# Optimization experiments

Hardware: AMD Instinct MI355X
Metric: run time of the kernel (lower is better)

Reference implementation:

```python
import jax, jax.numpy as jnp
import numpy as np

NUM_USERS = 100000
NUM_ITEMS = 50000
N_TOTAL = NUM_USERS + NUM_ITEMS
NNZ = 4000000
LATENT_DIM = 64
N_LAYERS = 3
BATCH = 16384


def setup_inputs() -> dict:
    key = jax.random.key(0)
    k1, k2, k3, k4, k5, k6, k7 = jax.random.split(key, 7)
    return {
        "user_emb": jax.random.normal(k1, (NUM_USERS, LATENT_DIM), dtype=jnp.float32) * 0.1,
        "item_emb": jax.random.normal(k2, (NUM_ITEMS, LATENT_DIM), dtype=jnp.float32) * 0.1,
        "vals": jax.random.uniform(k3, (NNZ,), dtype=jnp.float32),
        "rows": jax.random.randint(k4, (NNZ,), 0, N_TOTAL, dtype=jnp.int32),
        "cols": jax.random.randint(k5, (NNZ,), 0, N_TOTAL, dtype=jnp.int32),
        "users": jax.random.randint(k6, (BATCH,), 0, NUM_USERS, dtype=jnp.int64),
        "items": jax.random.randint(k7, (BATCH,), 0, NUM_ITEMS, dtype=jnp.int64),
    }


def _spmm(vals, rows, cols, x):
    # sparse.mm(A, x) with A given as COO edge list: out[r] += vals * x[c]
    return jax.ops.segment_sum(vals[:, None] * x[cols], rows, num_segments=N_TOTAL)


def reference(user_emb, item_emb, vals, rows, cols, users, items):
    # LightGCN.computer(): multi-hop propagation + mean over layer outputs
    all_emb = jnp.concatenate([user_emb, item_emb], axis=0)  # [N+M, d]
    acc = all_emb
    emb = all_emb
    for _ in range(N_LAYERS):
        emb = _spmm(vals, rows, cols, emb)
        acc = acc + emb
    light_out = acc / jnp.asarray(N_LAYERS + 1, dtype=acc.dtype)
    all_users = light_out[:NUM_USERS]
    all_items = light_out[NUM_USERS:]
    # forward(users, items): gather and elementwise dot product
    u = all_users[users]  # [B, d]
    i = all_items[items]  # [B, d]
    gamma = jnp.sum(u * i, axis=1)  # [B]
    return gamma
```

## Files before the change

kernel.cpp:

```cpp
#include <hip/hip_runtime.h>

#define NUM_USERS 100000
#define NUM_ITEMS 50000
#define N_TOTAL   150000
#define LATENT    64
#define BATCH     16384
#define BROWS     512
#define NB        293

typedef unsigned int u32;
typedef unsigned short u16;

__device__ __forceinline__ u16 f32_to_bf16(float f) {
    u32 u = __float_as_uint(f);
    u32 r = (u + 0x7FFFu + ((u >> 16) & 1u)) >> 16;
    return (u16)r;
}
__device__ __forceinline__ float bf16_lo(u32 w) { return __uint_as_float(w << 16); }
__device__ __forceinline__ float bf16_hi(u32 w) { return __uint_as_float(w & 0xFFFF0000u); }

__global__ void coarse_hist_kernel(const int* __restrict__ rows, int* __restrict__ ccnt, int nnz) {
    __shared__ int h[NB];
    for (int i = threadIdx.x; i < NB; i += blockDim.x) h[i] = 0;
    __syncthreads();
    int stride = gridDim.x * blockDim.x;
    for (int e = blockIdx.x * blockDim.x + threadIdx.x; e < nnz; e += stride)
        atomicAdd(&h[rows[e] >> 9], 1);
    __syncthreads();
    for (int i = threadIdx.x; i < NB; i += blockDim.x)
        if (h[i]) atomicAdd(&ccnt[i], h[i]);
}

__global__ void coarse_scan_kernel(const int* __restrict__ ccnt, int* __restrict__ cptr,
                                   int* __restrict__ ccur, int* __restrict__ rowptr, int nnz) {
    __shared__ int s[512];
    int t = threadIdx.x;
    int v = (t < NB) ? ccnt[t] : 0;
    s[t] = v;
    __syncthreads();
    for (int d = 1; d < 512; d <<= 1) {
        int x = (t >= d) ? s[t - d] : 0;
        __syncthreads();
        s[t] += x;
        __syncthreads();
    }
    int excl = s[t] - v;
    if (t < NB) { cptr[t] = excl; ccur[t] = excl; }
    if (t == 0) { cptr[NB] = nnz; rowptr[N_TOTAL] = nnz; }
}

__global__ void partition1_kernel(const int* __restrict__ rows, const int* __restrict__ cols,
                                  const float* __restrict__ vals,
                                  int* __restrict__ ccur, uint2* __restrict__ packed0, int nnz) {
    __shared__ int lh[NB];
    __shared__ int lc[NB];
    int t = threadIdx.x;
    for (int i = t; i < NB; i += blockDim.x) lh[i] = 0;
    __syncthreads();
    int epb = (nnz + gridDim.x - 1) / gridDim.x;
    int s0 = blockIdx.x * epb;
    int s1 = s0 + epb; if (s1 > nnz) s1 = nnz;
    for (int e = s0 + t; e < s1; e += blockDim.x)
        atomicAdd(&lh[rows[e] >> 9], 1);
    __syncthreads();
    for (int i = t; i < NB; i += blockDim.x) {
        int c = lh[i];
        lc[i] = c ? atomicAdd(&ccur[i], c) : 0;
    }
    __syncthreads();
    for (int e = s0 + t; e < s1; e += blockDim.x) {
        int r = rows[e];
        int pos = atomicAdd(&lc[r >> 9], 1);
        packed0[pos] = make_uint2((u32)cols[e] | ((u32)(r & (BROWS - 1)) << 18),
                                  __float_as_uint(vals[e]));
    }
}

__global__ void __launch_bounds__(BROWS)
partition2_kernel(const int* __restrict__ cptr, const uint2* __restrict__ packed0,
                  uint2* __restrict__ edges, int* __restrict__ rowptr) {
    __shared__ int cnt[BROWS];
    __shared__ int s[BROWS];
    __shared__ int cur[BROWS];
    int b = blockIdx.x;
    int t = threadIdx.x;
    int seg0 = cptr[b], seg1 = cptr[b + 1];
    cnt[t] = 0;
    __syncthreads();
    for (int i = seg0 + t; i < seg1; i += 2 * BROWS) {
        u32 k0 = packed0[i].x >> 18;
        int i2 = i + BROWS;
        if (i2 < seg1) {
            u32 k1 = packed0[i2].x >> 18;
            atomicAdd(&cnt[k0], 1);
            atomicAdd(&cnt[k1], 1);
        } else {
            atomicAdd(&cnt[k0], 1);
        }
    }
    __syncthreads();
    int v = cnt[t];
    s[t] = v;
    __syncthreads();
    for (int d = 1; d < BROWS; d <<= 1) {
        int x = (t >= d) ? s[t - d] : 0;
        __syncthreads();
        s[t] += x;
        __syncthreads();
    }
    int excl = s[t] - v;
    cur[t] = excl;
    int r = (b << 9) + t;
    if (r < N_TOTAL) rowptr[r] = seg0 + excl;
    __syncthreads();
    for (int i = seg0 + t; i < seg1; i += 2 * BROWS) {
        uint2 p0 = packed0[i];
        int i2 = i + BROWS;
        if (i2 < seg1) {
            uint2 p1 = packed0[i2];
            int pos0 = seg0 + atomicAdd(&cur[p0.x >> 18], 1);
            int pos1 = seg0 + atomicAdd(&cur[p1.x >> 18], 1);
            edges[pos0] = make_uint2(p0.x & 0x3FFFFu, p0.y);
            edges[pos1] = make_uint2(p1.x & 0x3FFFFu, p1.y);
        } else {
            int pos0 = seg0 + atomicAdd(&cur[p0.x >> 18], 1);
            edges[pos0] = make_uint2(p0.x & 0x3FFFFu, p0.y);
        }
    }
}

__global__ void convert_kernel(const float* __restrict__ ue, const float* __restrict__ ie,
                               u16* __restrict__ x) {
    int i = blockIdx.x * blockDim.x + threadIdx.x;
    if (i >= N_TOTAL * LATENT) return;
    float f = (i < NUM_USERS * LATENT) ? ue[i] : ie[i - NUM_USERS * LATENT];
    x[i] = f32_to_bf16(f);
}

__device__ __forceinline__ void spmm_row(const uint2* __restrict__ edges,
                                         const u16* __restrict__ x,
                                         int s, int e, int lane, float acc[4]) {
    int j = lane >> 4;
    int q = (lane & 15) << 2;
    acc[0] = acc[1] = acc[2] = acc[3] = 0.f;
    int i = s;
    for (; i + 16 <= e; i += 16) {
        uint2 e0 = edges[i + j];
        uint2 e1 = edges[i + 4 + j];
        uint2 e2 = edges[i + 8 + j];
        uint2 e3 = edges[i + 12 + j];
        uint2 x0 = *reinterpret_cast<const uint2*>(x + (size_t)e0.x * LATENT + q);
        uint2 x1 = *reinterpret_cast<const uint2*>(x + (size_t)e1.x * LATENT + q);
        uint2 x2 = *reinterpret_cast<const uint2*>(x + (size_t)e2.x * LATENT + q);
        uint2 x3 = *reinterpret_cast<const uint2*>(x + (size_t)e3.x * LATENT + q);
        float v0 = __uint_as_float(e0.y);
        float v1 = __uint_as_float(e1.y);
        float v2 = __uint_as_float(e2.y);
        float v3 = __uint_as_float(e3.y);
        acc[0] = fmaf(v0, bf16_lo(x0.x), acc[0]);
        acc[1] = fmaf(v0, bf16_hi(x0.x), acc[1]);
        acc[2] = fmaf(v0, bf16_lo(x0.y), acc[2]);
        acc[3] = fmaf(v0, bf16_hi(x0.y), acc[3]);
        acc[0] = fmaf(v1, bf16_lo(x1.x), acc[0]);
        acc[1] = fmaf(v1, bf16_hi(x1.x), acc[1]);
        acc[2] = fmaf(v1, bf16_lo(x1.y), acc[2]);
        acc[3] = fmaf(v1, bf16_hi(x1.y), acc[3]);
        acc[0] = fmaf(v2, bf16_lo(x2.x), acc[0]);
        acc[1] = fmaf(v2, bf16_hi(x2.x), acc[1]);
        acc[2] = fmaf(v2, bf16_lo(x2.y), acc[2]);
        acc[3] = fmaf(v2, bf16_hi(x2.y), acc[3]);
        acc[0] = fmaf(v3, bf16_lo(x3.x), acc[0]);
        acc[1] = fmaf(v3, bf16_hi(x3.x), acc[1]);
        acc[2] = fmaf(v3, bf16_lo(x3.y), acc[2]);
        acc[3] = fmaf(v3, bf16_hi(x3.y), acc[3]);
    }
    for (; i + 8 <= e; i += 8) {
        uint2 e0 = edges[i + j];
        uint2 e1 = edges[i + 4 + j];
        uint2 x0 = *reinterpret_cast<const uint2*>(x + (size_t)e0.x * LATENT + q);
        uint2 x1 = *reinterpret_cast<const uint2*>(x + (size_t)e1.x * LATENT + q);
        float v0 = __uint_as_float(e0.y);
        float v1 = __uint_as_float(e1.y);
        acc[0] = fmaf(v0, bf16_lo(x0.x), acc[0]);
        acc[1] = fmaf(v0, bf16_hi(x0.x), acc[1]);
        acc[2] = fmaf(v0, bf16_lo(x0.y), acc[2]);
        acc[3] = fmaf(v0, bf16_hi(x0.y), acc[3]);
        acc[0] = fmaf(v1, bf16_lo(x1.x), acc[0]);
        acc[1] = fmaf(v1, bf16_hi(x1.x), acc[1]);
        acc[2] = fmaf(v1, bf16_lo(x1.y), acc[2]);
        acc[3] = fmaf(v1, bf16_hi(x1.y), acc[3]);
    }
    for (; i < e; i += 4) {
        uint2 e0 = edges[i + j];
        float v0 = (i + j < e) ? __uint_as_float(e0.y) : 0.f;
        uint2 x0 = *reinterpret_cast<const uint2*>(x + (size_t)e0.x * LATENT + q);
        acc[0] = fmaf(v0, bf16_lo(x0.x), acc[0]);
        acc[1] = fmaf(v0, bf16_hi(x0.x), acc[1]);
        acc[2] = fmaf(v0, bf16_lo(x0.y), acc[2]);
        acc[3] = fmaf(v0, bf16_hi(x0.y), acc[3]);
    }
    #pragma unroll
    for (int k = 0; k < 4; ++k) {
        acc[k] += __shfl_xor(acc[k], 16, 64);
        acc[k] += __shfl_xor(acc[k], 32, 64);
    }
}

__global__ void spmm_kernel(const int* __restrict__ rowptr, const uint2* __restrict__ edges,
                            const u16* __restrict__ x, u16* __restrict__ y) {
    int row = blockIdx.x * 4 + (threadIdx.x >> 6);
    int lane = threadIdx.x & 63;
    int s = rowptr[row], e = rowptr[row + 1];
    float acc[4];
    spmm_row(edges, x, s, e, lane, acc);
    if (lane < 16) {
        u32 w0 = (u32)f32_to_bf16(acc[0]) | ((u32)f32_to_bf16(acc[1]) << 16);
        u32 w1 = (u32)f32_to_bf16(acc[2]) | ((u32)f32_to_bf16(acc[3]) << 16);
        *reinterpret_cast<uint2*>(y + (size_t)row * LATENT + (lane << 2)) = make_uint2(w0, w1);
    }
}

__global__ void spmm_batch_kernel(const int* __restrict__ rowptr, const uint2* __restrict__ edges,
                                  const u16* __restrict__ x,
                                  const int* __restrict__ users, const int* __restrict__ items,
                                  float* __restrict__ u_acc, float* __restrict__ i_acc) {
    int slot = blockIdx.x * 4 + (threadIdx.x >> 6);
    int lane = threadIdx.x & 63;
    int row = (slot < BATCH) ? users[slot] : (NUM_USERS + items[slot - BATCH]);
    int s = rowptr[row], e = rowptr[row + 1];
    float acc[4];
    spmm_row(edges, x, s, e, lane, acc);
    if (lane < 16) {
        float* dst = (slot < BATCH) ? (u_acc + (size_t)slot * LATENT)
                                    : (i_acc + (size_t)(slot - BATCH) * LATENT);
        float4* p = reinterpret_cast<float4*>(dst + (lane << 2));
        float4 old = *p;
        *p = make_float4(old.x + acc[0], old.y + acc[1], old.z + acc[2], old.w + acc[3]);
    }
}

__global__ void init_acc_kernel(const float* __restrict__ user_emb,
                                const float* __restrict__ item_emb,
                                const int* __restrict__ users,
                                const int* __restrict__ items,
                                float* __restrict__ u_acc,
                                float* __restrict__ i_acc) {
    int tid = blockIdx.x * blockDim.x + threadIdx.x;
    int b = tid >> 6, d = tid & 63;
    if (b >= BATCH) return;
    u_acc[tid] = user_emb[(size_t)users[b] * LATENT + d];
    i_acc[tid] = item_emb[(size_t)items[b] * LATENT + d];
}

__global__ void gather_acc_kernel(const u16* __restrict__ emb,
                                  const int* __restrict__ users,
                                  const int* __restrict__ items,
                                  float* __restrict__ u_acc,
                                  float* __restrict__ i_acc) {
    int tid = blockIdx.x * blockDim.x + threadIdx.x;
    int b = tid >> 6, d = tid & 63;
    if (b >= BATCH) return;
    u_acc[tid] += __uint_as_float(((u32)emb[(size_t)users[b] * LATENT + d]) << 16);
    i_acc[tid] += __uint_as_float(((u32)emb[((size_t)items[b] + NUM_USERS) * LATENT + d]) << 16);
}

__global__ void dot_kernel(const float* __restrict__ u_acc,
                           const float* __restrict__ i_acc,
                           float* __restrict__ out) {
    int b = blockIdx.x;
    int d = threadIdx.x;
    float p = u_acc[b * 64 + d] * i_acc[b * 64 + d];
    #pragma unroll
    for (int off = 32; off; off >>= 1) p += __shfl_down(p, off, 64);
    if (d == 0) out[b] = p * (1.0f / 16.0f);
}

extern "C" void kernel_launch(void* const* d_in, const int* in_sizes, int n_in,
                              void* d_out, int out_size, void* d_ws, size_t ws_size,
                              hipStream_t stream) {
    const float* user_emb = (const float*)d_in[0];
    const float* item_emb = (const float*)d_in[1];
    const float* vals     = (const float*)d_in[2];
    const int*   rows     = (const int*)d_in[3];
    const int*   cols     = (const int*)d_in[4];
    const int*   users    = (const int*)d_in[5];
    const int*   items    = (const int*)d_in[6];
    float* out = (float*)d_out;

    const int nnz = in_sizes[2];

    char* ws = (char*)d_ws;
    const size_t embB  = (size_t)N_TOTAL * LATENT * sizeof(u16);
    const size_t accB  = (size_t)BATCH * LATENT * sizeof(float);
    const size_t edgeB = (size_t)(nnz + 16) * sizeof(uint2);

    size_t off = 0;
    u16*   emb_a   = (u16*)  (ws + off); off += embB;
    u16*   emb_b   = (u16*)  (ws + off); off += embB;
    uint2* packed0 = (uint2*)(ws + off); off += edgeB;
    uint2* edges   = (uint2*)(ws + off); off += edgeB;
    float* u_acc   = (float*)(ws + off); off += accB;
    float* i_acc   = (float*)(ws + off); off += accB;
    int*   rowptr  = (int*)  (ws + off); off += (size_t)(N_TOTAL + 1) * sizeof(int);
    int*   ccnt    = (int*)  (ws + off); off += (size_t)(NB + 1) * sizeof(int);
    int*   cptr    = (int*)  (ws + off); off += (size_t)(NB + 1) * sizeof(int);
    int*   ccur    = (int*)  (ws + off); off += (size_t)(NB + 1) * sizeof(int);

    hipMemsetAsync(ccnt, 0, (size_t)(NB + 1) * sizeof(int), stream);
    hipMemsetAsync(edges + nnz, 0, 16 * sizeof(uint2), stream);
    coarse_hist_kernel<<<512, 512, 0, stream>>>(rows, ccnt, nnz);
    coarse_scan_kernel<<<1, 512, 0, stream>>>(ccnt, cptr, ccur, rowptr, nnz);
    partition1_kernel<<<512, 512, 0, stream>>>(rows, cols, vals, ccur, packed0, nnz);
    partition2_kernel<<<NB, BROWS, 0, stream>>>(cptr, packed0, edges, rowptr);

    convert_kernel<<<(N_TOTAL * LATENT + 255) / 256, 256, 0, stream>>>(user_emb, item_emb, emb_a);
    init_acc_kernel<<<(BATCH * 64) / 256, 256, 0, stream>>>(
        user_emb, item_emb, users, items, u_acc, i_acc);

    u16* cur = emb_a;
    u16* nxt = emb_b;
    for (int l = 0; l < 2; ++l) {
        spmm_kernel<<<N_TOTAL / 4, 256, 0, stream>>>(rowptr, edges, cur, nxt);
        gather_acc_kernel<<<(BATCH * 64) / 256, 256, 0, stream>>>(
            nxt, users, items, u_acc, i_acc);
        u16* t = cur; cur = nxt; nxt = t;
    }

    spmm_batch_kernel<<<(2 * BATCH) / 4, 256, 0, stream>>>(
        rowptr, edges, cur, users, items, u_acc, i_acc);

    dot_kernel<<<BATCH, 64, 0, stream>>>(u_acc, i_acc, out);
}
```

Baseline: 345.8 us.

## Stage partition1 edges in shared memory to coalesce scattered global writes

```diff
diff --git a/kernel.cpp b/kernel.cpp
--- a/kernel.cpp
+++ b/kernel.cpp
@@ -7,6 +7,8 @@
 #define BATCH     16384
 #define BROWS     512
 #define NB        293
+#define P1_T      512
+#define P1_C      4096
 
 typedef unsigned int u32;
 typedef unsigned short u16;
@@ -49,30 +51,73 @@
     if (t == 0) { cptr[NB] = nnz; rowptr[N_TOTAL] = nnz; }
 }
 
-__global__ void partition1_kernel(const int* __restrict__ rows, const int* __restrict__ cols,
-                                  const float* __restrict__ vals,
-                                  int* __restrict__ ccur, uint2* __restrict__ packed0, int nnz) {
-    __shared__ int lh[NB];
-    __shared__ int lc[NB];
+__global__ void __launch_bounds__(P1_T)
+partition1_kernel(const int* __restrict__ rows, const int* __restrict__ cols,
+                  const float* __restrict__ vals,
+                  int* __restrict__ ccur, uint2* __restrict__ packed0, int nnz) {
+    __shared__ u32 skey[P1_C];
+    __shared__ u32 sval[P1_C];
+    __shared__ u16 sbucket[P1_C];
+    __shared__ int cnt[NB];
+    __shared__ int lstart[NB];
+    __shared__ int lcur[NB];
+    __shared__ int gbase[NB];
+    __shared__ int scanbuf[P1_T];
+
     int t = threadIdx.x;
-    for (int i = t; i < NB; i += blockDim.x) lh[i] = 0;
-    __syncthreads();
-    int epb = (nnz + gridDim.x - 1) / gridDim.x;
-    int s0 = blockIdx.x * epb;
-    int s1 = s0 + epb; if (s1 > nnz) s1 = nnz;
-    for (int e = s0 + t; e < s1; e += blockDim.x)
-        atomicAdd(&lh[rows[e] >> 9], 1);
-    __syncthreads();
-    for (int i = t; i < NB; i += blockDim.x) {
-        int c = lh[i];
-        lc[i] = c ? atomicAdd(&ccur[i], c) : 0;
-    }
-    __syncthreads();
-    for (int e = s0 + t; e < s1; e += blockDim.x) {
-        int r = rows[e];
-        int pos = atomicAdd(&lc[r >> 9], 1);
-        packed0[pos] = make_uint2((u32)cols[e] | ((u32)(r & (BROWS - 1)) << 18),
-                                  __float_as_uint(vals[e]));
+    int base = blockIdx.x * P1_C;
+    int chunkN = nnz - base; if (chunkN > P1_C) chunkN = P1_C;
+
+    for (int i = t; i < NB; i += P1_T) cnt[i] = 0;
+    __syncthreads();
+
+    int   er[8]; u32 ek[8]; u32 ev[8];
+    #pragma unroll
+    for (int k = 0; k < 8; ++k) {
+        int e = base + k * P1_T + t;
+        bool ok = (k * P1_T + t) < chunkN;
+        int r = ok ? rows[e] : 0;
+        er[k] = ok ? (r >> 9) : -1;
+        if (ok) {
+            ek[k] = (u32)cols[e] | ((u32)(r & (BROWS - 1)) << 18);
+            ev[k] = __float_as_uint(vals[e]);
+            atomicAdd(&cnt[er[k]], 1);
+        }
+    }
+    __syncthreads();
+
+    int v = (t < NB) ? cnt[t] : 0;
+    scanbuf[t] = v;
+    __syncthreads();
+    for (int d = 1; d < P1_T; d <<= 1) {
+        int x = (t >= d) ? scanbuf[t - d] : 0;
+        __syncthreads();
+        scanbuf[t] += x;
+        __syncthreads();
+    }
+    if (t < NB) {
+        int excl = scanbuf[t] - v;
+        lstart[t] = excl;
+        lcur[t] = excl;
+        gbase[t] = v ? atomicAdd(&ccur[t], v) : 0;
+    }
+    __syncthreads();
+
+    #pragma unroll
+    for (int k = 0; k < 8; ++k) {
+        if (er[k] >= 0) {
+            int pos = atomicAdd(&lcur[er[k]], 1);
+            skey[pos] = ek[k];
+            sval[pos] = ev[k];
+            sbucket[pos] = (u16)er[k];
+        }
+    }
+    __syncthreads();
+
+    for (int idx = t; idx < chunkN; idx += P1_T) {
+        int b2 = sbucket[idx];
+        int gp = gbase[b2] + (idx - lstart[b2]);
+        packed0[gp] = make_uint2(skey[idx], sval[idx]);
     }
 }
 
@@ -310,7 +355,8 @@
     hipMemsetAsync(edges + nnz, 0, 16 * sizeof(uint2), stream);
     coarse_hist_kernel<<<512, 512, 0, stream>>>(rows, ccnt, nnz);
     coarse_scan_kernel<<<1, 512, 0, stream>>>(ccnt, cptr, ccur, rowptr, nnz);
-    partition1_kernel<<<512, 512, 0, stream>>>(rows, cols, vals, ccur, packed0, nnz);
+    partition1_kernel<<<(nnz + P1_C - 1) / P1_C, P1_T, 0, stream>>>(
+        rows, cols, vals, ccur, packed0, nnz);
     partition2_kernel<<<NB, BROWS, 0, stream>>>(cptr, packed0, edges, rowptr);
 
     convert_kernel<<<(N_TOTAL * LATENT + 255) / 256, 256, 0, stream>>>(user_emb, item_emb, emb_a);
```

Result: faster. 336.4 us (-2.7%).
